# Optimization experiments

Measured on AMD Instinct MI355X. Metric: run time of the kernel, lower is better.

Reference implementation:

```python
import jax, jax.numpy as jnp
import numpy as np

B, C, H, W = 8, 256, 64, 64
C8 = C // 8


def setup_inputs() -> dict:
    key = jax.random.key(0)
    ks = jax.random.split(key, 8)
    scale = 0.05
    return {
        "x": jax.random.normal(ks[0], (B, C, H, W), jnp.float32),
        "Wf": jax.random.normal(ks[1], (C8, C), jnp.float32) * scale,
        "bf": jax.random.normal(ks[2], (C8,), jnp.float32) * scale,
        "Wg": jax.random.normal(ks[3], (C8, C), jnp.float32) * scale,
        "bg": jax.random.normal(ks[4], (C8,), jnp.float32) * scale,
        "Wh": jax.random.normal(ks[5], (C, C), jnp.float32) * scale,
        "bh": jax.random.normal(ks[6], (C,), jnp.float32) * scale,
        "gamma": jax.random.normal(ks[7], (1,), jnp.float32) * scale,
    }


def reference(x, Wf, bf, Wg, bg, Wh, bh, gamma):
    b, c, h, w = x.shape
    n = h * w
    xr = x.reshape(b, c, n)  # flatten spatial: [B, C, N]
    # 1x1 convs == per-pixel linear projections
    f = jnp.einsum('oc,bcn->bon', Wf, xr) + bf[None, :, None]  # [B, C/8, N]
    g = jnp.einsum('oc,bcn->bon', Wg, xr) + bg[None, :, None]  # [B, C/8, N]
    hh = jnp.einsum('oc,bcn->bon', Wh, xr) + bh[None, :, None]  # [B, C, N]
    # s = f^T @ g : unscaled attention logits, [B, N, N]
    s = jnp.einsum('bki,bkj->bij', f, g)
    attention = jax.nn.softmax(s, axis=-1)
    # out = h @ attention^T : out[b,c,i] = sum_j h[b,c,j] * attn[b,i,j]
    out = jnp.einsum('bcj,bij->bci', hh, attention)
    out = out.reshape(b, c, w, h)  # original code uses (W, H); H==W here
    out = gamma[0] * out + x
    return (out, attention)
```

## Files before the change

### kernel.cpp

```cpp
#include <hip/hip_runtime.h>
#include <hip/hip_bf16.h>

typedef unsigned short u16;
typedef __attribute__((ext_vector_type(8))) short short8;
typedef __attribute__((ext_vector_type(4))) float f32x4;

#define BATCH 8
#define CH 256
#define NPIX 4096
#define KD 32

static __device__ __forceinline__ u16 f2bf(float f) {
  union { __hip_bfloat16 h; u16 u; } cv;
  cv.h = __float2bfloat16(f);
  return cv.u;
}

__global__ __launch_bounds__(256) void proj_kernel(
    const float* __restrict__ x,
    const float* __restrict__ Wf, const float* __restrict__ bfp,
    const float* __restrict__ Wg, const float* __restrict__ bgp,
    const float* __restrict__ Wh, const float* __restrict__ bhp,
    u16* __restrict__ fT, u16* __restrict__ gT, u16* __restrict__ hhb)
{
  __shared__ float xs[CH][36];
  const int b  = blockIdx.x >> 7;
  const int n0 = (blockIdx.x & 127) * 32;
  const int t  = threadIdx.x;

  const float* xb = x + ((size_t)b * CH) * NPIX + n0;
  #pragma unroll
  for (int kk = 0; kk < 8; ++kk) {
    int v = kk * 256 + t;
    int c = v >> 3, p4 = v & 7;
    float4 d = *(const float4*)(xb + (size_t)c * NPIX + p4 * 4);
    *(float4*)&xs[c][p4 * 4] = d;
  }
  __syncthreads();

  const int o = t;
  float acch[32];
  #pragma unroll
  for (int p = 0; p < 32; ++p) acch[p] = bhp[o];

  const int o2 = t & 63;
  const int oo = o2 & 31;
  const bool isf = o2 < 32;
  const float* Wfg = isf ? Wf : Wg;
  const float bias2 = isf ? bfp[oo] : bgp[oo];
  const int pg = (t >> 6) * 8;
  float accf[8];
  #pragma unroll
  for (int p = 0; p < 8; ++p) accf[p] = bias2;

  const float* whr  = Wh  + o * CH;
  const float* wfgr = Wfg + oo * CH;
  for (int c = 0; c < CH; c += 4) {
    float4 wh4 = *(const float4*)(whr + c);
    float4 wf4 = *(const float4*)(wfgr + c);
    float wha[4] = {wh4.x, wh4.y, wh4.z, wh4.w};
    float wfa[4] = {wf4.x, wf4.y, wf4.z, wf4.w};
    #pragma unroll
    for (int cc = 0; cc < 4; ++cc) {
      float wh = wha[cc], wf = wfa[cc];
      #pragma unroll
      for (int p4 = 0; p4 < 8; ++p4) {
        float4 xv = *(const float4*)&xs[c + cc][p4 * 4];
        acch[p4*4+0] = fmaf(wh, xv.x, acch[p4*4+0]);
        acch[p4*4+1] = fmaf(wh, xv.y, acch[p4*4+1]);
        acch[p4*4+2] = fmaf(wh, xv.z, acch[p4*4+2]);
        acch[p4*4+3] = fmaf(wh, xv.w, acch[p4*4+3]);
      }
      #pragma unroll
      for (int p = 0; p < 8; ++p) accf[p] = fmaf(wf, xs[c + cc][pg + p], accf[p]);
    }
  }

  u16* hrow = hhb + ((size_t)b * CH + o) * NPIX + n0;
  #pragma unroll
  for (int q = 0; q < 4; ++q) {
    uint4 u;
    u.x = f2bf(acch[q*8+0]) | ((unsigned)f2bf(acch[q*8+1]) << 16);
    u.y = f2bf(acch[q*8+2]) | ((unsigned)f2bf(acch[q*8+3]) << 16);
    u.z = f2bf(acch[q*8+4]) | ((unsigned)f2bf(acch[q*8+5]) << 16);
    u.w = f2bf(acch[q*8+6]) | ((unsigned)f2bf(acch[q*8+7]) << 16);
    *(uint4*)(hrow + q * 8) = u;
  }
  u16* dst = (isf ? fT : gT) + ((size_t)b * NPIX + n0 + pg) * KD + oo;
  #pragma unroll
  for (int p = 0; p < 8; ++p) dst[(size_t)p * KD] = f2bf(accf[p]);
}

__global__ __launch_bounds__(512, 4) void fused_attn_pv(
    const u16* __restrict__ fT, const u16* __restrict__ gT,
    const u16* __restrict__ hhb, const float* __restrict__ x,
    const float* __restrict__ gamma,
    float* __restrict__ attn_out, float* __restrict__ outp)
{
  __shared__ u16 Pt[2][64 * 64];
  __shared__ float part[8][64];
  __shared__ float invs[64];

  const int bid = blockIdx.x;
  const int b  = bid & 7;
  const int n0 = (bid >> 3) * 64;
  const int t  = threadIdx.x;
  const int iw = t >> 6, l = t & 63;
  const int lg = l >> 4, lm = l & 15;

  const u16* fb = fT + ((size_t)b * NPIX + n0) * KD;
  const u16* gb = gT + (size_t)b * NPIX * KD;
  const u16* hb = hhb + (size_t)b * CH * NPIX;

  f32x4 z4 = {0.f, 0.f, 0.f, 0.f};

  short8 ff[4];
  #pragma unroll
  for (int it = 0; it < 4; ++it)
    ff[it] = *(const short8*)(fb + (it * 16 + lm) * KD + lg * 8);

  float sum[4][4];
  #pragma unroll
  for (int it = 0; it < 4; ++it)
    #pragma unroll
    for (int r = 0; r < 4; ++r) sum[it][r] = 0.f;

  const int j1 = iw * 512;
  for (int jt = 0; jt < 32; ++jt) {
    int j0 = j1 + jt * 16;
    short8 gf = *(const short8*)(gb + (size_t)(j0 + lm) * KD + lg * 8);
    #pragma unroll
    for (int it = 0; it < 4; ++it) {
      f32x4 s = __builtin_amdgcn_mfma_f32_16x16x32_bf16(ff[it], gf, z4, 0, 0, 0);
      #pragma unroll
      for (int r = 0; r < 4; ++r) sum[it][r] += __expf(s[r]);
    }
  }
  #pragma unroll
  for (int m = 1; m < 16; m <<= 1)
    #pragma unroll
    for (int it = 0; it < 4; ++it)
      #pragma unroll
      for (int r = 0; r < 4; ++r) sum[it][r] += __shfl_xor(sum[it][r], m, 64);
  if (lm == 0) {
    #pragma unroll
    for (int it = 0; it < 4; ++it)
      #pragma unroll
      for (int r = 0; r < 4; ++r) part[iw][it * 16 + lg * 4 + r] = sum[it][r];
  }
  __syncthreads();
  if (t < 64) {
    float s = 0.f;
    #pragma unroll
    for (int w2 = 0; w2 < 8; ++w2) s += part[w2][t];
    invs[t] = 1.0f / s;
  }
  __syncthreads();

  const int it2 = iw >> 1, jsub = iw & 1;
  float inv4[4];
  #pragma unroll
  for (int r = 0; r < 4; ++r) inv4[r] = invs[it2 * 16 + lg * 4 + r];
  const short8 f2 = ff[it2];

  float* arow = attn_out + ((size_t)b * NPIX + n0 + it2 * 16 + lg * 4) * NPIX;

  f32x4 acc[2][4];
  #pragma unroll
  for (int mf = 0; mf < 2; ++mf)
    #pragma unroll
    for (int nf = 0; nf < 4; ++nf) acc[mf][nf] = z4;

  short8 gP[2], gQ[2], hP[2][2], hQ[2][2];

  auto LDG = [&](short8 (&g2)[2], short8 (&h2)[2][2], int JC) {
    #pragma unroll
    for (int st = 0; st < 2; ++st)
      g2[st] = *(const short8*)(gb + (size_t)(JC + jsub * 32 + st * 16 + lm) * KD + lg * 8);
    #pragma unroll
    for (int m = 0; m < 2; ++m)
      #pragma unroll
      for (int ks = 0; ks < 2; ++ks)
        h2[m][ks] = *(const short8*)(hb + (size_t)(iw * 32 + m * 16 + lm) * NPIX
                                     + JC + ks * 32 + lg * 8);
  };

  auto HALF = [&](u16* buf, short8 (&gc)[2], short8 (&hc)[2][2],
                  short8 (&gn)[2], short8 (&hn)[2][2], int JC, int JN) {
    f32x4 s[2];
    #pragma unroll
    for (int st = 0; st < 2; ++st)
      s[st] = __builtin_amdgcn_mfma_f32_16x16x32_bf16(f2, gc[st], z4, 0, 0, 0);
    LDG(gn, hn, JN);
    #pragma unroll
    for (int st = 0; st < 2; ++st) {
      const int j0 = JC + jsub * 32 + st * 16;
      #pragma unroll
      for (int r = 0; r < 4; ++r) {
        float p = __expf(s[st][r]) * inv4[r];
        __builtin_nontemporal_store(p, arow + (size_t)r * NPIX + j0 + lm);
        int iloc = it2 * 16 + lg * 4 + r;
        int jloc = jsub * 32 + st * 16 + lm;
        int byte = iloc * 128 + ((jloc * 2) ^ (((lg * 4 + r) & 7) << 4));
        *(u16*)((char*)buf + byte) = f2bf(p);
      }
    }
    asm volatile("s_waitcnt lgkmcnt(0)\n\ts_barrier" ::: "memory");
    #pragma unroll
    for (int nf = 0; nf < 4; ++nf) {
      #pragma unroll
      for (int ks = 0; ks < 2; ++ks) {
        int byte = (nf * 16 + lm) * 128 + (((ks * 4 + lg) * 16) ^ ((lm & 7) << 4));
        short8 pf = *(const short8*)((char*)buf + byte);
        acc[0][nf] = __builtin_amdgcn_mfma_f32_16x16x32_bf16(hc[0][ks], pf, acc[0][nf], 0, 0, 0);
        acc[1][nf] = __builtin_amdgcn_mfma_f32_16x16x32_bf16(hc[1][ks], pf, acc[1][nf], 0, 0, 0);
      }
    }
  };

  LDG(gP, hP, 0);
  for (int jc = 0; jc < NPIX; jc += 128) {
    int n1 = (jc + 64) & (NPIX - 1);
    int n2 = (jc + 128) & (NPIX - 1);
    HALF(&Pt[0][0], gP, hP, gQ, hQ, jc, n1);
    HALF(&Pt[1][0], gQ, hQ, gP, hP, jc + 64, n2);
  }

  const float gm = gamma[0];
  #pragma unroll
  for (int mf = 0; mf < 2; ++mf) {
    #pragma unroll
    for (int r = 0; r < 4; ++r) {
      int c = iw * 32 + mf * 16 + lg * 4 + r;
      #pragma unroll
      for (int nf = 0; nf < 4; ++nf) {
        int i = n0 + nf * 16 + lm;
        size_t idx = ((size_t)b * CH + c) * NPIX + i;
        outp[idx] = fmaf(gm, acc[mf][nf][r], x[idx]);
      }
    }
  }
}

extern "C" void kernel_launch(void* const* d_in, const int* in_sizes, int n_in,
                              void* d_out, int out_size, void* d_ws, size_t ws_size,
                              hipStream_t stream) {
  const float* x     = (const float*)d_in[0];
  const float* Wf    = (const float*)d_in[1];
  const float* bf    = (const float*)d_in[2];
  const float* Wg    = (const float*)d_in[3];
  const float* bg    = (const float*)d_in[4];
  const float* Wh    = (const float*)d_in[5];
  const float* bh    = (const float*)d_in[6];
  const float* gamma = (const float*)d_in[7];

  float* outp = (float*)d_out;
  float* attn_out = outp + (size_t)BATCH * CH * NPIX;

  u16* fT = (u16*)d_ws;
  u16* gT = fT + (size_t)BATCH * NPIX * KD;
  u16* hh = gT + (size_t)BATCH * NPIX * KD;

  proj_kernel<<<dim3(BATCH * (NPIX / 32)), dim3(256), 0, stream>>>(
      x, Wf, bf, Wg, bg, Wh, bh, fT, gT, hh);

  fused_attn_pv<<<dim3(BATCH * (NPIX / 64)), dim3(512), 0, stream>>>(
      fT, gT, hh, x, gamma, attn_out, outp);
}
```

Baseline: 326.6 us.

## Warp-specialize attention PV loop into producer and consumer waves

Splits the eight waves of the fused attention kernel into four producer waves, which compute QK logits, exp, normalization, attention stores and the LDS P tile, and four consumer waves, which load h and run the PV MFMAs at raised priority. Producers fill one LDS buffer while consumers read the other, with barriers between stages. The goal is to overlap the exp and attention-store work with the PV matrix multiplies. In exchange, only half the waves issue MFMAs, consumers hold a larger accumulator set (16 f32x4), h loads are no longer prefetched a stage ahead, and the work may become unbalanced between the two roles.

```diff
diff --git a/kernel.cpp b/kernel.cpp
--- a/kernel.cpp
+++ b/kernel.cpp
@@ -157,86 +157,91 @@
   }
   __syncthreads();
 
-  const int it2 = iw >> 1, jsub = iw & 1;
+  const bool isprod = (iw < 4);
+  const int pw = iw & 3;
+
   float inv4[4];
   #pragma unroll
-  for (int r = 0; r < 4; ++r) inv4[r] = invs[it2 * 16 + lg * 4 + r];
-  const short8 f2 = ff[it2];
-
-  float* arow = attn_out + ((size_t)b * NPIX + n0 + it2 * 16 + lg * 4) * NPIX;
-
-  f32x4 acc[2][4];
-  #pragma unroll
-  for (int mf = 0; mf < 2; ++mf)
-    #pragma unroll
-    for (int nf = 0; nf < 4; ++nf) acc[mf][nf] = z4;
-
-  short8 gP[2], gQ[2], hP[2][2], hQ[2][2];
-
-  auto LDG = [&](short8 (&g2)[2], short8 (&h2)[2][2], int JC) {
-    #pragma unroll
-    for (int st = 0; st < 2; ++st)
-      g2[st] = *(const short8*)(gb + (size_t)(JC + jsub * 32 + st * 16 + lm) * KD + lg * 8);
-    #pragma unroll
-    for (int m = 0; m < 2; ++m)
-      #pragma unroll
-      for (int ks = 0; ks < 2; ++ks)
-        h2[m][ks] = *(const short8*)(hb + (size_t)(iw * 32 + m * 16 + lm) * NPIX
-                                     + JC + ks * 32 + lg * 8);
+  for (int r = 0; r < 4; ++r) inv4[r] = invs[pw * 16 + lg * 4 + r];
+  const short8 f2 = ff[pw];
+  float* abase = attn_out + ((size_t)b * NPIX + n0 + pw * 16) * NPIX;
+
+  const u16* hbase = hb + (size_t)(pw * 64 + lm) * NPIX + lg * 8;
+
+  f32x4 acc[4][4];
+  if (!isprod) {
+    #pragma unroll
+    for (int a = 0; a < 4; ++a)
+      #pragma unroll
+      for (int c2 = 0; c2 < 4; ++c2) acc[a][c2] = z4;
+  }
+
+  auto PRODUCE = [&](u16* buf, int JC) {
+    short8 g4[4];
+    #pragma unroll
+    for (int st = 0; st < 4; ++st)
+      g4[st] = *(const short8*)(gb + (size_t)(JC + st * 16 + lm) * KD + lg * 8);
+    #pragma unroll
+    for (int st = 0; st < 4; ++st) {
+      f32x4 s = __builtin_amdgcn_mfma_f32_16x16x32_bf16(f2, g4[st], z4, 0, 0, 0);
+      #pragma unroll
+      for (int r = 0; r < 4; ++r) {
+        float p = __expf(s[r]) * inv4[r];
+        __builtin_nontemporal_store(
+            p, abase + (size_t)(lg * 4 + r) * NPIX + JC + st * 16 + lm);
+        int iloc = pw * 16 + lg * 4 + r;
+        int byte = iloc * 128 + (((st * 16 + lm) * 2) ^ ((iloc & 7) << 4));
+        *(u16*)((char*)buf + byte) = f2bf(p);
+      }
+    }
   };
 
-  auto HALF = [&](u16* buf, short8 (&gc)[2], short8 (&hc)[2][2],
-                  short8 (&gn)[2], short8 (&hn)[2][2], int JC, int JN) {
-    f32x4 s[2];
-    #pragma unroll
-    for (int st = 0; st < 2; ++st)
-      s[st] = __builtin_amdgcn_mfma_f32_16x16x32_bf16(f2, gc[st], z4, 0, 0, 0);
-    LDG(gn, hn, JN);
-    #pragma unroll
-    for (int st = 0; st < 2; ++st) {
-      const int j0 = JC + jsub * 32 + st * 16;
+  auto CONSUME = [&](const u16* buf, int JC) {
+    #pragma unroll
+    for (int ks = 0; ks < 2; ++ks) {
+      short8 h[4];
+      #pragma unroll
+      for (int ct = 0; ct < 4; ++ct)
+        h[ct] = *(const short8*)(hbase + (size_t)(ct * 16) * NPIX + JC + ks * 32);
+      __builtin_amdgcn_s_setprio(1);
+      #pragma unroll
+      for (int nf = 0; nf < 4; ++nf) {
+        int byte = (nf * 16 + lm) * 128 + (((ks * 4 + lg) * 16) ^ ((lm & 7) << 4));
+        short8 pfr = *(const short8*)((const char*)buf + byte);
+        #pragma unroll
+        for (int ct = 0; ct < 4; ++ct)
+          acc[ct][nf] = __builtin_amdgcn_mfma_f32_16x16x32_bf16(
+              h[ct], pfr, acc[ct][nf], 0, 0, 0);
+      }
+      __builtin_amdgcn_s_setprio(0);
+    }
+  };
+
+  if (isprod) PRODUCE(&Pt[0][0], 0);
+  __syncthreads();
+
+  for (int jc = 0; jc < NPIX; jc += 128) {
+    if (isprod) PRODUCE(&Pt[1][0], jc + 64);
+    else        CONSUME(&Pt[0][0], jc);
+    asm volatile("s_waitcnt lgkmcnt(0)\n\ts_barrier" ::: "memory");
+    if (isprod) { if (jc + 128 < NPIX) PRODUCE(&Pt[0][0], jc + 128); }
+    else        CONSUME(&Pt[1][0], jc + 64);
+    asm volatile("s_waitcnt lgkmcnt(0)\n\ts_barrier" ::: "memory");
+  }
+
+  if (!isprod) {
+    const float gm = gamma[0];
+    #pragma unroll
+    for (int ct = 0; ct < 4; ++ct) {
       #pragma unroll
       for (int r = 0; r < 4; ++r) {
-        float p = __expf(s[st][r]) * inv4[r];
-        __builtin_nontemporal_store(p, arow + (size_t)r * NPIX + j0 + lm);
-        int iloc = it2 * 16 + lg * 4 + r;
-        int jloc = jsub * 32 + st * 16 + lm;
-        int byte = iloc * 128 + ((jloc * 2) ^ (((lg * 4 + r) & 7) << 4));
-        *(u16*)((char*)buf + byte) = f2bf(p);
-      }
-    }
-    asm volatile("s_waitcnt lgkmcnt(0)\n\ts_barrier" ::: "memory");
-    #pragma unroll
-    for (int nf = 0; nf < 4; ++nf) {
-      #pragma unroll
-      for (int ks = 0; ks < 2; ++ks) {
-        int byte = (nf * 16 + lm) * 128 + (((ks * 4 + lg) * 16) ^ ((lm & 7) << 4));
-        short8 pf = *(const short8*)((char*)buf + byte);
-        acc[0][nf] = __builtin_amdgcn_mfma_f32_16x16x32_bf16(hc[0][ks], pf, acc[0][nf], 0, 0, 0);
-        acc[1][nf] = __builtin_amdgcn_mfma_f32_16x16x32_bf16(hc[1][ks], pf, acc[1][nf], 0, 0, 0);
-      }
-    }
-  };
-
-  LDG(gP, hP, 0);
-  for (int jc = 0; jc < NPIX; jc += 128) {
-    int n1 = (jc + 64) & (NPIX - 1);
-    int n2 = (jc + 128) & (NPIX - 1);
-    HALF(&Pt[0][0], gP, hP, gQ, hQ, jc, n1);
-    HALF(&Pt[1][0], gQ, hQ, gP, hP, jc + 64, n2);
-  }
-
-  const float gm = gamma[0];
-  #pragma unroll
-  for (int mf = 0; mf < 2; ++mf) {
-    #pragma unroll
-    for (int r = 0; r < 4; ++r) {
-      int c = iw * 32 + mf * 16 + lg * 4 + r;
-      #pragma unroll
-      for (int nf = 0; nf < 4; ++nf) {
-        int i = n0 + nf * 16 + lm;
-        size_t idx = ((size_t)b * CH + c) * NPIX + i;
-        outp[idx] = fmaf(gm, acc[mf][nf][r], x[idx]);
+        int c = pw * 64 + ct * 16 + lg * 4 + r;
+        #pragma unroll
+        for (int nf = 0; nf < 4; ++nf) {
+          int i = n0 + nf * 16 + lm;
+          size_t idx = ((size_t)b * CH + c) * NPIX + i;
+          outp[idx] = fmaf(gm, acc[ct][nf][r], x[idx]);
+        }
       }
     }
   }
```

After: 381.7 us. 16.9% more time.
